# Optimization experiments

Measured on AMD Instinct MI355X. Metric: run time of the kernel, lower is better.

Reference implementation:

```python
import jax, jax.numpy as jnp
import numpy as np

G, S, DG, HN, HE, L, F = 64, 160, 128, 128, 16, 2, 16


def _rn(k, shape, scale=0.05):
    return jax.random.normal(k, shape, dtype=jnp.float32) * scale


def setup_inputs() -> dict:
    ks = jax.random.split(jax.random.key(0), 26)
    return {
        "gene_codes": jax.random.normal(ks[0], (G, DG), dtype=jnp.float32),
        "node_entry_w": _rn(ks[1], (HN, DG)), "node_entry_b": _rn(ks[2], (HN,)),
        "node_wih0": _rn(ks[3], (4 * HN, 1)), "node_wih": _rn(ks[4], (L - 1, 4 * HN, HN)),
        "node_whh": _rn(ks[5], (L, 4 * HN, HN)), "node_bih": _rn(ks[6], (L, 4 * HN)), "node_bhh": _rn(ks[7], (L, 4 * HN)),
        "node_exit_w": _rn(ks[8], (32, HN)), "node_exit_b": _rn(ks[9], (32,)),
        "edge_entry_w": _rn(ks[10], (HE, 32)), "edge_entry_b": _rn(ks[11], (HE,)),
        "edge_wih0": _rn(ks[12], (4 * HE, 1)), "edge_wih": _rn(ks[13], (L - 1, 4 * HE, HE)),
        "edge_whh": _rn(ks[14], (L, 4 * HE, HE)), "edge_bih": _rn(ks[15], (L, 4 * HE)), "edge_bhh": _rn(ks[16], (L, 4 * HE)),
        "ee1_w": _rn(ks[17], (8, HE)), "ee1_b": _rn(ks[18], (8,)),
        "ee2_w": _rn(ks[19], (2, 8)), "ee2_b": _rn(ks[20], (2,)),
        "ef1_w": _rn(ks[21], (8, HE)), "ef1_b": _rn(ks[22], (8,)),
        "ef2_w": _rn(ks[23], (2 * F, 8)), "ef2_b": _rn(ks[24], (2 * F,)),
        "graphs_size": S,
    }


def _lstm_zero_input(h0, wih0, wih, whh, bih, bhh, steps):
    # Multi-layer PyTorch-style LSTM (gate order i,f,g,o) whose input sequence is all-zeros
    # of feature size 1; h0 is replicated across layers (as in the original .repeat).
    nl = whh.shape[0]
    h = jnp.stack([h0] * nl)
    c = jnp.zeros_like(h)
    zero_in = jnp.zeros((h0.shape[0], 1), h0.dtype)

    def step(carry, _):
        h, c = carry
        hs, cs = [], []
        inp = zero_in
        for l in range(nl):
            w_in = wih0 if l == 0 else wih[l - 1]
            gates = inp @ w_in.T + h[l] @ whh[l].T + bih[l] + bhh[l]
            i, f, g, o = jnp.split(gates, 4, axis=-1)
            cn = jax.nn.sigmoid(f) * c[l] + jax.nn.sigmoid(i) * jnp.tanh(g)
            hn = jax.nn.sigmoid(o) * jnp.tanh(cn)
            hs.append(hn); cs.append(cn)
            inp = hn
        return (jnp.stack(hs), jnp.stack(cs)), hs[-1]

    _, outs = jax.lax.scan(step, (h, c), None, length=steps)
    return outs  # [steps, B, H] top-layer hiddens


def reference(gene_codes, node_entry_w, node_entry_b, node_wih0, node_wih, node_whh, node_bih, node_bhh, node_exit_w, node_exit_b, edge_entry_w, edge_entry_b, edge_wih0, edge_wih, edge_whh, edge_bih, edge_bhh, ee1_w, ee1_b, ee2_w, ee2_b, ef1_w, ef1_b, ef2_w, ef2_b, graphs_size):
    s_len = int(graphs_size)
    g_n = gene_codes.shape[0]
    n_max = s_len + 1
    m = s_len * g_n  # total node steps == number of edge sequences
    fdim = ef2_w.shape[0] // 2

    # node RNN over zero inputs, h0 from gene codes
    h0n = jax.nn.relu(gene_codes @ node_entry_w.T + node_entry_b)
    node_out = _lstm_zero_input(h0n, node_wih0, node_wih, node_whh, node_bih, node_bhh, s_len)  # [S,G,HN]
    # uniform graph sizes: torch's flipped packed data == reversed step-major layout,
    # flat index k -> (step = S-1-k//G, graph = k%G)
    node_flat = jnp.flip(node_out, axis=0).reshape(m, -1)

    # edge RNN: one sequence per node step; zero inputs, so full-length run gives
    # identical hiddens at every valid packed step
    h0e = jax.nn.relu(jax.nn.relu(node_flat @ node_exit_w.T + node_exit_b) @ edge_entry_w.T + edge_entry_b)
    eh = _lstm_zero_input(h0e, edge_wih0, edge_wih, edge_whh, edge_bih, edge_bhh, s_len)  # [S,M,HE]

    e = jax.nn.sigmoid(jax.nn.relu(eh @ ee1_w.T + ee1_b) @ ee2_w.T + ee2_b)          # [S,M,2]
    f = (jax.nn.relu(eh @ ef1_w.T + ef1_b) @ ef2_w.T + ef2_b).reshape(s_len, m, 2, fdim)

    # ragged index construction: edge sequence k has row = edges_size[k] = S - k//G,
    # graph id = k%G, valid steps s < row, column = s
    k = jnp.arange(m)
    gid = k % g_n
    row = s_len - k // g_n
    s = jnp.arange(s_len)[:, None]
    mask = (s < row[None, :]).reshape(-1)
    gid2 = jnp.broadcast_to(gid[None, :], (s_len, m)).reshape(-1)
    row2 = jnp.broadcast_to(row[None, :], (s_len, m)).reshape(-1)
    col2 = jnp.broadcast_to(s, (s_len, m)).reshape(-1)

    el = jnp.where(mask, e[..., 0].reshape(-1), 0.0)
    eu = jnp.where(mask, e[..., 1].reshape(-1), 0.0)
    exist = jnp.zeros((g_n, n_max, n_max), gene_codes.dtype)
    exist = exist.at[gid2, row2, col2].add(el).at[gid2, col2, row2].add(eu)

    fl = jnp.where(mask[:, None], f[:, :, 0, :].reshape(-1, fdim), 0.0)
    fu = jnp.where(mask[:, None], f[:, :, 1, :].reshape(-1, fdim), 0.0)
    feat = jnp.zeros((g_n, n_max, n_max, fdim), gene_codes.dtype)
    feat = feat.at[gid2, row2, col2].add(fl).at[gid2, col2, row2].add(fu)
    return exist, feat
```

## Files before the change

### kernel.cpp

```cpp
#include <hip/hip_runtime.h>


typedef __attribute__((ext_vector_type(8))) short short8;
typedef __attribute__((ext_vector_type(4))) short short4v;
typedef __attribute__((ext_vector_type(4))) float floatx4;
typedef _Float16 half2v __attribute__((ext_vector_type(2)));

#define NG 64
#define NMAX 161
#define CH 16
#define NCH 10

__device__ __forceinline__ float sgm(float x) {
  return __builtin_amdgcn_rcpf(1.0f + __expf(-x));
}
__device__ __forceinline__ float tanhf_(float x) {
  return 2.0f * __builtin_amdgcn_rcpf(1.0f + __expf(-2.0f * x)) - 1.0f;
}
__device__ __forceinline__ unsigned short f2b(float x) {
  union { float f; unsigned u; } v; v.f = x;
  unsigned r = v.u + 0x7fffu + ((v.u >> 16) & 1u);
  return (unsigned short)(r >> 16);
}
__device__ __forceinline__ float b2f(unsigned short h) {
  union { unsigned u; float f; } v; v.u = ((unsigned)h) << 16; return v.f;
}
__device__ __forceinline__ half2v pkh(float a, float b) {
  return __builtin_bit_cast(half2v, __builtin_amdgcn_cvt_pkrtz(a, b));
}
__device__ __forceinline__ void barrier_lds() {
  asm volatile("s_waitcnt lgkmcnt(0)" ::: "memory");
  __builtin_amdgcn_s_barrier();
}

#define RORF(x, N) __builtin_bit_cast(float, __builtin_amdgcn_update_dpp(      \
    __builtin_bit_cast(int, (x)), __builtin_bit_cast(int, (x)),                \
    0x120 | (N), 0xF, 0xF, false))

__device__ __forceinline__ void rotpack(float h, half2v* out) {
  const float r1  = RORF(h, 1),  r2  = RORF(h, 2),  r3  = RORF(h, 3);
  const float r4  = RORF(h, 4),  r5  = RORF(h, 5),  r6  = RORF(h, 6);
  const float r7  = RORF(h, 7),  r8  = RORF(h, 8),  r9  = RORF(h, 9);
  const float r10 = RORF(h, 10), r11 = RORF(h, 11), r12 = RORF(h, 12);
  const float r13 = RORF(h, 13), r14 = RORF(h, 14), r15 = RORF(h, 15);
  out[0] = pkh(h,   r1);
  out[1] = pkh(r2,  r3);
  out[2] = pkh(r4,  r5);
  out[3] = pkh(r6,  r7);
  out[4] = pkh(r8,  r9);
  out[5] = pkh(r10, r11);
  out[6] = pkh(r12, r13);
  out[7] = pkh(r14, r15);
}

__global__ __launch_bounds__(512) void node_fused(
    const float* __restrict__ gene,
    const float* __restrict__ entw,
    const float* __restrict__ entb,
    const float* __restrict__ nwih,
    const float* __restrict__ nwhh,
    const float* __restrict__ nbih,
    const float* __restrict__ nbhh,
    unsigned short* __restrict__ h0w,
    unsigned short* __restrict__ X3,
    unsigned short* __restrict__ nflat,
    int* __restrict__ flag0, int* __restrict__ flag1)
{
  __shared__ __align__(16) unsigned short hA[2][16][136];
  __shared__ __align__(16) unsigned short s_b[128][136];

  const int tid  = threadIdx.x;
  const int role = blockIdx.x >> 2;
  const int rb4  = blockIdx.x & 3;
  const int wv   = tid >> 6;
  const int lane = tid & 63;
  const int lo   = lane & 15;
  const int hi   = lane >> 4;

  if (role == 0) {
    const int nb = rb4;
    const int u  = (wv << 4) | lo;

    short8 B0[4][4];
#pragma unroll
    for (int t = 0; t < 4; ++t) {
      const int n = t * 128 + u;
#pragma unroll
      for (int ks = 0; ks < 4; ++ks) {
        const float* src = nwhh + n * 128 + ks * 32 + hi * 8;
        short8 bfr;
#pragma unroll
        for (int jj = 0; jj < 8; ++jj) bfr[jj] = (short)f2b(src[jj]);
        B0[t][ks] = bfr;
      }
    }
    const float bi0 = nbih[u]       + nbhh[u];
    const float bf0 = nbih[128 + u] + nbhh[128 + u];
    const float bg0 = nbih[256 + u] + nbhh[256 + u];
    const float bo0 = nbih[384 + u] + nbhh[384 + u];

    {
      const int q  = tid >> 5;
      const int u4 = (tid & 31) * 4;
      const float* gc = gene + (nb * 16 + q) * 128;
      float acc[4] = { entb[u4], entb[u4 + 1], entb[u4 + 2], entb[u4 + 3] };
      for (int qq = 0; qq < 32; ++qq) {
        const float4 gv = *(const float4*)&gc[qq * 4];
#pragma unroll
        for (int r = 0; r < 4; ++r) {
          const float4 wv2 = *(const float4*)&entw[(u4 + r) * 128 + qq * 4];
          acc[r] += gv.x * wv2.x + gv.y * wv2.y + gv.z * wv2.z + gv.w * wv2.w;
        }
      }
#pragma unroll
      for (int r = 0; r < 4; ++r)
        hA[0][q][u4 + r] = f2b(fmaxf(acc[r], 0.0f));
    }

    float c0[4] = {0.f, 0.f, 0.f, 0.f};
    __syncthreads();

    for (int c = 0; c < NCH; ++c) {
      for (int tt = 0; tt < CH; ++tt) {
        const int t  = c * CH + tt;
        const int rb = t & 1, wb = rb ^ 1;
        floatx4 a0 = {bi0, bi0, bi0, bi0};
        floatx4 a1 = {bf0, bf0, bf0, bf0};
        floatx4 a2 = {bg0, bg0, bg0, bg0};
        floatx4 a3 = {bo0, bo0, bo0, bo0};
        const unsigned short* ar = &hA[rb][lo][hi * 8];
#pragma unroll
        for (int ks = 0; ks < 4; ++ks) {
          const short8 afr = *(const short8*)(ar + ks * 32);
          a0 = __builtin_amdgcn_mfma_f32_16x16x32_bf16(afr, B0[0][ks], a0, 0, 0, 0);
          a1 = __builtin_amdgcn_mfma_f32_16x16x32_bf16(afr, B0[1][ks], a1, 0, 0, 0);
          a2 = __builtin_amdgcn_mfma_f32_16x16x32_bf16(afr, B0[2][ks], a2, 0, 0, 0);
          a3 = __builtin_amdgcn_mfma_f32_16x16x32_bf16(afr, B0[3][ks], a3, 0, 0, 0);
        }
        const size_t obase = (size_t)(t * 64 + nb * 16) * 128;
#pragma unroll
        for (int r = 0; r < 4; ++r) {
          const float iv = sgm(a0[r]);
          const float fv = sgm(a1[r]);
          const float gv = tanhf_(a2[r]);
          const float ov = sgm(a3[r]);
          const float cn = fv * c0[r] + iv * gv;
          c0[r] = cn;
          const unsigned short hb = f2b(ov * tanhf_(cn));
          const int q = hi * 4 + r;
          hA[wb][q][u] = hb;
          __builtin_nontemporal_store(hb, &h0w[obase + (size_t)q * 128 + u]);
        }
        if (tt < CH - 1) barrier_lds();
      }
      __syncthreads();
      if (tid == 0) {
        __threadfence();
        __hip_atomic_fetch_add(&flag0[c], 1, __ATOMIC_RELEASE,
                               __HIP_MEMORY_SCOPE_AGENT);
      }
    }

  } else if (role == 1) {
    const int xg = rb4;
    for (int i = tid; i < 128 * 32; i += 512) {
      const int nc = i >> 5, k4 = (i & 31) * 4;
      const float4 w = *(const float4*)&nwih[(size_t)(xg * 128 + nc) * 128 + k4];
      s_b[nc][k4]     = f2b(w.x);
      s_b[nc][k4 + 1] = f2b(w.y);
      s_b[nc][k4 + 2] = f2b(w.z);
      s_b[nc][k4 + 3] = f2b(w.w);
    }
    const int gg = wv & 3;
    const int ch = wv >> 2;

    for (int c = 0; c < NCH; ++c) {
      if (tid == 0) {
        while (__hip_atomic_load(&flag0[c], __ATOMIC_ACQUIRE,
                                 __HIP_MEMORY_SCOPE_AGENT) < 4)
          __builtin_amdgcn_s_sleep(8);
        __threadfence();
      }
      __syncthreads();

      for (int tt = 0; tt < CH; ++tt) {
        const int t = c * CH + tt;
        floatx4 acc[4];
#pragma unroll
        for (int nt = 0; nt < 4; ++nt) acc[nt] = (floatx4){0.f, 0.f, 0.f, 0.f};
        const unsigned short* arow =
            h0w + (size_t)(t * 64 + gg * 16 + lo) * 128 + hi * 8;
#pragma unroll
        for (int ks = 0; ks < 4; ++ks) {
          const short8 afr = *(const short8*)(arow + ks * 32);
#pragma unroll
          for (int nt = 0; nt < 4; ++nt) {
            const short8 bfr =
                *(const short8*)&s_b[ch * 64 + nt * 16 + lo][ks * 32 + hi * 8];
            acc[nt] = __builtin_amdgcn_mfma_f32_16x16x32_bf16(afr, bfr, acc[nt], 0, 0, 0);
          }
        }
#pragma unroll
        for (int nt = 0; nt < 4; ++nt) {
          const size_t base3 =
              ((((size_t)gg * 160 + t) * 512) + xg * 128 + ch * 64 + nt * 16 + lo) * 16
              + hi * 4;
          short4v xv;
#pragma unroll
          for (int r = 0; r < 4; ++r) xv[r] = (short)f2b(acc[nt][r]);
          __builtin_nontemporal_store(xv, (short4v*)&X3[base3]);
        }
      }
      __syncthreads();
      if (tid == 0) {
        __threadfence();
        __hip_atomic_fetch_add(&flag1[c], 1, __ATOMIC_RELEASE,
                               __HIP_MEMORY_SCOPE_AGENT);
      }
    }

  } else {
    const int nb = rb4;
    const int u  = (wv << 4) | lo;

    short8 B1[4][4];
#pragma unroll
    for (int t = 0; t < 4; ++t) {
      const int n = t * 128 + u;
#pragma unroll
      for (int ks = 0; ks < 4; ++ks) {
        const float* src = nwhh + 512 * 128 + n * 128 + ks * 32 + hi * 8;
        short8 bfr;
#pragma unroll
        for (int jj = 0; jj < 8; ++jj) bfr[jj] = (short)f2b(src[jj]);
        B1[t][ks] = bfr;
      }
    }
    const float bi1 = nbih[512 + u]       + nbhh[512 + u];
    const float bf1 = nbih[512 + 128 + u] + nbhh[512 + 128 + u];
    const float bg1 = nbih[512 + 256 + u] + nbhh[512 + 256 + u];
    const float bo1 = nbih[512 + 384 + u] + nbhh[512 + 384 + u];

    {
      const int q  = tid >> 5;
      const int u4 = (tid & 31) * 4;
      const float* gc = gene + (nb * 16 + q) * 128;
      float acc[4] = { entb[u4], entb[u4 + 1], entb[u4 + 2], entb[u4 + 3] };
      for (int qq = 0; qq < 32; ++qq) {
        const float4 gv = *(const float4*)&gc[qq * 4];
#pragma unroll
        for (int r = 0; r < 4; ++r) {
          const float4 wv2 = *(const float4*)&entw[(u4 + r) * 128 + qq * 4];
          acc[r] += gv.x * wv2.x + gv.y * wv2.y + gv.z * wv2.z + gv.w * wv2.w;
        }
      }
#pragma unroll
      for (int r = 0; r < 4; ++r)
        hA[0][q][u4 + r] = f2b(fmaxf(acc[r], 0.0f));
    }

    float c1[4] = {0.f, 0.f, 0.f, 0.f};
    const size_t xstep = 512 * 16;
    const unsigned short* xb = X3 + ((size_t)nb * 160) * xstep
                             + (size_t)u * 16 + hi * 4;
    __syncthreads();

    for (int c = 0; c < NCH; ++c) {
      if (tid == 0) {
        while (__hip_atomic_load(&flag1[c], __ATOMIC_ACQUIRE,
                                 __HIP_MEMORY_SCOPE_AGENT) < 4)
          __builtin_amdgcn_s_sleep(8);
        __threadfence();
      }
      __syncthreads();

      const unsigned short* xp = xb + (size_t)(c * CH) * xstep;
      short4v x0 = *(const short4v*)(xp);
      short4v x1 = *(const short4v*)(xp + 128 * 16);
      short4v x2 = *(const short4v*)(xp + 256 * 16);
      short4v x3 = *(const short4v*)(xp + 384 * 16);

      for (int tt = 0; tt < CH; ++tt) {
        const int t  = c * CH + tt;
        const int rb = t & 1, wb = rb ^ 1;

        floatx4 a0 = {bi1, bi1, bi1, bi1};
        floatx4 a1 = {bf1, bf1, bf1, bf1};
        floatx4 a2 = {bg1, bg1, bg1, bg1};
        floatx4 a3 = {bo1, bo1, bo1, bo1};
        const unsigned short* ar = &hA[rb][lo][hi * 8];
#pragma unroll
        for (int ks = 0; ks < 4; ++ks) {
          const short8 afr = *(const short8*)(ar + ks * 32);
          a0 = __builtin_amdgcn_mfma_f32_16x16x32_bf16(afr, B1[0][ks], a0, 0, 0, 0);
          a1 = __builtin_amdgcn_mfma_f32_16x16x32_bf16(afr, B1[1][ks], a1, 0, 0, 0);
          a2 = __builtin_amdgcn_mfma_f32_16x16x32_bf16(afr, B1[2][ks], a2, 0, 0, 0);
          a3 = __builtin_amdgcn_mfma_f32_16x16x32_bf16(afr, B1[3][ks], a3, 0, 0, 0);
        }

        const short4v cx0 = x0, cx1 = x1, cx2 = x2, cx3 = x3;
        if (tt + 1 < CH) {
          const unsigned short* xn = xb + (size_t)(t + 1) * xstep;
          x0 = *(const short4v*)(xn);
          x1 = *(const short4v*)(xn + 128 * 16);
          x2 = *(const short4v*)(xn + 256 * 16);
          x3 = *(const short4v*)(xn + 384 * 16);
        }

        const size_t obase = (size_t)((159 - t) * 64 + nb * 16) * 128;
#pragma unroll
        for (int r = 0; r < 4; ++r) {
          const float iv = sgm(a0[r] + b2f((unsigned short)cx0[r]));
          const float fv = sgm(a1[r] + b2f((unsigned short)cx1[r]));
          const float gv = tanhf_(a2[r] + b2f((unsigned short)cx2[r]));
          const float ov = sgm(a3[r] + b2f((unsigned short)cx3[r]));
          const float cn = fv * c1[r] + iv * gv;
          c1[r] = cn;
          const unsigned short hb = f2b(ov * tanhf_(cn));
          const int q = hi * 4 + r;
          hA[wb][q][u] = hb;
          __builtin_nontemporal_store(hb, &nflat[obase + (size_t)q * 128 + u]);
        }
        barrier_lds();
      }
    }
  }
}

__global__ __launch_bounds__(256, 1) void edge_kernel(
    const unsigned short* __restrict__ nflat,
    const float* __restrict__ exw, const float* __restrict__ exb,
    const float* __restrict__ enw, const float* __restrict__ enb,
    const float* __restrict__ ewih,
    const float* __restrict__ ewhh,
    const float* __restrict__ ebih, const float* __restrict__ ebhh,
    const float* __restrict__ ee1w, const float* __restrict__ ee1b,
    const float* __restrict__ ee2w, const float* __restrict__ ee2b,
    const float* __restrict__ ef1w, const float* __restrict__ ef1b,
    const float* __restrict__ ef2w, const float* __restrict__ ef2b,
    float* __restrict__ out)
{
  const int tid = threadIdx.x;
  const int sg  = tid >> 4;
  const int u   = tid & 15;
  const int b   = blockIdx.x;

  const int row = b >> 8, r = b & 255;
  const int bb  = (row == 1) ? (511 - r) : ((row << 8) + r);
  const int kbase = bb * 16;
  const int jrow  = 160 - (bb >> 2);
  const int gid   = (kbase & 63) + sg;

  __shared__ __align__(16) float s_nf[16][132];
  __shared__ float s_w0s[64][17];
  __shared__ float s_was[64][17];
  __shared__ float s_wbs[64][17];
  __shared__ float s_wh[16][17];
  __shared__ float s_ef2[32][10];
  __shared__ __align__(16) float s_ee2[16];
  __shared__ __align__(16) float t1b[16][12];
  __shared__ __align__(16) float t2b[16][12];
  __shared__ __align__(16) float x32[16][36];

  for (int i = tid; i < 16 * 128; i += 256)
    s_nf[i >> 7][i & 127] = b2f(nflat[(size_t)(kbase + (i >> 7)) * 128 + (i & 127)]);
  for (int i = tid; i < 64 * 16; i += 256) {
    s_w0s[i >> 4][i & 15] = ewhh[i];
    s_was[i >> 4][i & 15] = ewih[i];
    s_wbs[i >> 4][i & 15] = ewhh[1024 + i];
  }
  for (int i = tid; i < 8 * 16; i += 256) {
    s_wh[i >> 4][i & 15]       = ee1w[i];
    s_wh[8 + (i >> 4)][i & 15] = ef1w[i];
  }
  for (int i = tid; i < 32 * 8; i += 256) s_ef2[i >> 3][i & 7] = ef2w[i];
  if (tid < 16) s_ee2[tid] = ee2w[tid];

  if (b < NG) {
    for (int d = tid; d < NMAX; d += 256) {
      out[(size_t)b * (NMAX * NMAX) + (size_t)d * NMAX + d] = 0.0f;
      float* fb = out + (size_t)NG * NMAX * NMAX
                + ((size_t)b * NMAX * NMAX + (size_t)d * NMAX + d) * 16;
#pragma unroll
      for (int q = 0; q < 16; ++q) fb[q] = 0.0f;
    }
  }

  const float be0i = ebih[u]      + ebhh[u];
  const float be0f = ebih[16 + u] + ebhh[16 + u];
  const float be0g = ebih[32 + u] + ebhh[32 + u];
  const float be0o = ebih[48 + u] + ebhh[48 + u];
  const float be1i = ebih[64 + u]      + ebhh[64 + u];
  const float be1f = ebih[64 + 16 + u] + ebhh[64 + 16 + u];
  const float be1g = ebih[64 + 32 + u] + ebhh[64 + 32 + u];
  const float be1o = ebih[64 + 48 + u] + ebhh[64 + 48 + u];
  const float hbias = (u < 8) ? ee1b[u] : ef1b[u - 8];
  const float f2bl = ef2b[u], f2bu = ef2b[16 + u];
  const float e2bias = (u < 2) ? ee2b[u] : 0.0f;

  __syncthreads();

  half2v W0h[4][8], WAh[4][8], WBh[4][8], WHh[8];
#pragma unroll
  for (int g = 0; g < 4; ++g) {
    const int rw = g * 16 + u;
#pragma unroll
    for (int j = 0; j < 8; ++j) {
      const int v0 = (u + 2 * j) & 15, v1 = (u + 2 * j + 1) & 15;
      W0h[g][j] = pkh(s_w0s[rw][v0], s_w0s[rw][v1]);
      WAh[g][j] = pkh(s_was[rw][v0], s_was[rw][v1]);
      WBh[g][j] = pkh(s_wbs[rw][v0], s_wbs[rw][v1]);
    }
  }
#pragma unroll
  for (int j = 0; j < 8; ++j) {
    const int v0 = (u + 2 * j) & 15, v1 = (u + 2 * j + 1) & 15;
    WHh[j] = pkh(s_wh[u][v0], s_wh[u][v1]);
  }

  {
    float acc0 = exb[u], acc1 = exb[16 + u];
    const float* w0p = exw + u * 128;
    const float* w1p = exw + (16 + u) * 128;
    for (int qq = 0; qq < 32; ++qq) {
      const float4 nv  = *(const float4*)&s_nf[sg][qq * 4];
      const float4 w0v = *(const float4*)&w0p[qq * 4];
      const float4 w1v = *(const float4*)&w1p[qq * 4];
      acc0 += nv.x * w0v.x + nv.y * w0v.y + nv.z * w0v.z + nv.w * w0v.w;
      acc1 += nv.x * w1v.x + nv.y * w1v.y + nv.z * w1v.z + nv.w * w1v.w;
    }
    x32[sg][u] = fmaxf(acc0, 0.0f);
    x32[sg][16 + u] = fmaxf(acc1, 0.0f);
  }
  __builtin_amdgcn_wave_barrier();
  float c0 = 0.0f, c1 = 0.0f;
  half2v h20[8], h21[8];
  {
    float acc = enb[u];
    const float* ewp = enw + u * 32;
#pragma unroll
    for (int qq = 0; qq < 8; ++qq) {
      const float4 xv  = *(const float4*)&x32[sg][qq * 4];
      const float4 wv2 = *(const float4*)&ewp[qq * 4];
      acc += xv.x * wv2.x + xv.y * wv2.y + xv.z * wv2.z + xv.w * wv2.w;
    }
    const float h0e = fmaxf(acc, 0.0f);
    rotpack(h0e, h20);
#pragma unroll
    for (int j = 0; j < 8; ++j) h21[j] = h20[j];
  }

  float* exi = out + (size_t)gid * (NMAX * NMAX);
  float* fea = out + (size_t)NG * NMAX * NMAX + (size_t)gid * (NMAX * NMAX) * 16;
  const int jN = jrow * NMAX;

  for (int s = 0; s <= jrow; ++s) {
    const bool doStep = (s < jrow);
    const bool doHead = (s > 0);

    float a0, a1, a2, a3;
    if (doStep) {
      a0 = be0i; a1 = be0f; a2 = be0g; a3 = be0o;
#pragma unroll
      for (int j = 0; j < 8; ++j) {
        a0 = __builtin_amdgcn_fdot2(h20[j], W0h[0][j], a0, false);
        a1 = __builtin_amdgcn_fdot2(h20[j], W0h[1][j], a1, false);
        a2 = __builtin_amdgcn_fdot2(h20[j], W0h[2][j], a2, false);
        a3 = __builtin_amdgcn_fdot2(h20[j], W0h[3][j], a3, false);
      }
    }

    if (doHead) {
      __builtin_amdgcn_wave_barrier();
      const int sm = s - 1;
      const float2 ta0 = *(const float2*)&t2b[sg][0];
      const float2 ta1 = *(const float2*)&t2b[sg][2];
      const float2 ta2 = *(const float2*)&t2b[sg][4];
      const float2 ta3 = *(const float2*)&t2b[sg][6];
      const float2 wl0 = *(const float2*)&s_ef2[u][0];
      const float2 wl1 = *(const float2*)&s_ef2[u][2];
      const float2 wl2 = *(const float2*)&s_ef2[u][4];
      const float2 wl3 = *(const float2*)&s_ef2[u][6];
      const float2 wu0 = *(const float2*)&s_ef2[16 + u][0];
      const float2 wu1 = *(const float2*)&s_ef2[16 + u][2];
      const float2 wu2 = *(const float2*)&s_ef2[16 + u][4];
      const float2 wu3 = *(const float2*)&s_ef2[16 + u][6];
      const float fl = f2bl
          + ta0.x * wl0.x + ta0.y * wl0.y + ta1.x * wl1.x + ta1.y * wl1.y
          + ta2.x * wl2.x + ta2.y * wl2.y + ta3.x * wl3.x + ta3.y * wl3.y;
      const float fu = f2bu
          + ta0.x * wu0.x + ta0.y * wu0.y + ta1.x * wu1.x + ta1.y * wu1.y
          + ta2.x * wu2.x + ta2.y * wu2.y + ta3.x * wu3.x + ta3.y * wu3.y;
      fea[((size_t)jN + sm) * 16 + u] = fl;
      fea[((size_t)sm * NMAX + jrow) * 16 + u] = fu;
      if (u < 2) {
        const float4 t1a = *(const float4*)&t1b[sg][0];
        const float4 t1c = *(const float4*)&t1b[sg][4];
        const float4 we0 = *(const float4*)&s_ee2[u * 8];
        const float4 we1 = *(const float4*)&s_ee2[u * 8 + 4];
        float e = e2bias
            + t1a.x * we0.x + t1a.y * we0.y + t1a.z * we0.z + t1a.w * we0.w
            + t1c.x * we1.x + t1c.y * we1.y + t1c.z * we1.z + t1c.w * we1.w;
        const size_t idx = (u == 0) ? ((size_t)jN + sm)
                                    : ((size_t)sm * NMAX + jrow);
        exi[idx] = sgm(e);
      }
    }

    if (doStep) {
      {
        const float iv = sgm(a0), fv = sgm(a1), gv = tanhf_(a2), ov = sgm(a3);
        c0 = fv * c0 + iv * gv;
        rotpack(ov * tanhf_(c0), h20);
      }
      float b0 = be1i, b1 = be1f, b2 = be1g, b3 = be1o;
#pragma unroll
      for (int j = 0; j < 8; ++j) {
        b0 = __builtin_amdgcn_fdot2(h20[j], WAh[0][j], b0, false);
        b1 = __builtin_amdgcn_fdot2(h20[j], WAh[1][j], b1, false);
        b2 = __builtin_amdgcn_fdot2(h20[j], WAh[2][j], b2, false);
        b3 = __builtin_amdgcn_fdot2(h20[j], WAh[3][j], b3, false);
      }
#pragma unroll
      for (int j = 0; j < 8; ++j) {
        b0 = __builtin_amdgcn_fdot2(h21[j], WBh[0][j], b0, false);
        b1 = __builtin_amdgcn_fdot2(h21[j], WBh[1][j], b1, false);
        b2 = __builtin_amdgcn_fdot2(h21[j], WBh[2][j], b2, false);
        b3 = __builtin_amdgcn_fdot2(h21[j], WBh[3][j], b3, false);
      }
      {
        const float iv = sgm(b0), fv = sgm(b1), gv = tanhf_(b2), ov = sgm(b3);
        c1 = fv * c1 + iv * gv;
        rotpack(ov * tanhf_(c1), h21);
      }
      {
        float th = hbias;
#pragma unroll
        for (int j = 0; j < 8; ++j)
          th = __builtin_amdgcn_fdot2(h21[j], WHh[j], th, false);
        th = fmaxf(th, 0.0f);
        if (u < 8) t1b[sg][u] = th; else t2b[sg][u - 8] = th;
      }
      __builtin_amdgcn_wave_barrier();
    }
  }
}

extern "C" void kernel_launch(void* const* d_in, const int* in_sizes, int n_in,
                              void* d_out, int out_size, void* d_ws, size_t ws_size,
                              hipStream_t stream) {
  (void)in_sizes; (void)n_in; (void)out_size; (void)ws_size;
  const float* gene = (const float*)d_in[0];
  const float* entw = (const float*)d_in[1];
  const float* entb = (const float*)d_in[2];
  const float* nwih = (const float*)d_in[4];
  const float* nwhh = (const float*)d_in[5];
  const float* nbih = (const float*)d_in[6];
  const float* nbhh = (const float*)d_in[7];
  const float* exw  = (const float*)d_in[8];
  const float* exb  = (const float*)d_in[9];
  const float* enw  = (const float*)d_in[10];
  const float* enb  = (const float*)d_in[11];
  const float* ewih = (const float*)d_in[13];
  const float* ewhh = (const float*)d_in[14];
  const float* ebih = (const float*)d_in[15];
  const float* ebhh = (const float*)d_in[16];
  const float* ee1w = (const float*)d_in[17];
  const float* ee1b = (const float*)d_in[18];
  const float* ee2w = (const float*)d_in[19];
  const float* ee2b = (const float*)d_in[20];
  const float* ef1w = (const float*)d_in[21];
  const float* ef1b = (const float*)d_in[22];
  const float* ef2w = (const float*)d_in[23];
  const float* ef2b = (const float*)d_in[24];

  char* ws = (char*)d_ws;
  unsigned short* nflat = (unsigned short*)(ws);
  unsigned short* h0w   = (unsigned short*)(ws + 2621440);
  int* flag0            = (int*)(ws + 5242880);
  int* flag1            = (int*)(ws + 5242880 + 4096);
  unsigned short* X3    = (unsigned short*)(ws + 5259264);

  hipMemsetAsync(ws + 5242880, 0, 8192, stream);
  node_fused<<<12, 512, 0, stream>>>(gene, entw, entb, nwih, nwhh, nbih, nbhh,
                                     h0w, X3, nflat, flag0, flag1);
  edge_kernel<<<640, 256, 0, stream>>>(nflat, exw, exb, enw, enb, ewih, ewhh,
                                       ebih, ebhh, ee1w, ee1b, ee2w, ee2b,
                                       ef1w, ef1b, ef2w, ef2b, (float*)d_out);
}
```

Baseline: 459.0 us.

## Fuse layer-1 input projection into layer-0 recurrence blocks, drop middle role

Each layer-0 block now keeps the full layer-1 input weight matrix in LDS (about 136 KB). After each step it multiplies its fresh hidden state by that matrix and writes X3 directly. This removes the intermediate h0 buffer, the separate projection role and one stage of cross-block flag handoff. The layer-1 blocks now wait on a per-block counter instead of a per-chunk counter. In exchange, the layer-0 recurrence does extra MFMA work and a barrier on its serial critical path every step, and the large LDS allocation limits occupancy.

New measurement: 456.4 us. No clear change (-0.6%).

```diff
diff --git a/kernel.cpp b/kernel.cpp
--- a/kernel.cpp
+++ b/kernel.cpp
@@ -61,25 +61,34 @@
     const float* __restrict__ nwhh,
     const float* __restrict__ nbih,
     const float* __restrict__ nbhh,
-    unsigned short* __restrict__ h0w,
     unsigned short* __restrict__ X3,
     unsigned short* __restrict__ nflat,
-    int* __restrict__ flag0, int* __restrict__ flag1)
+    int* __restrict__ flagP)
 {
-  __shared__ __align__(16) unsigned short hA[2][16][136];
-  __shared__ __align__(16) unsigned short s_b[128][136];
-
   const int tid  = threadIdx.x;
   const int role = blockIdx.x >> 2;
-  const int rb4  = blockIdx.x & 3;
+  const int nb   = blockIdx.x & 3;
   const int wv   = tid >> 6;
   const int lane = tid & 63;
   const int lo   = lane & 15;
   const int hi   = lane >> 4;
 
+  if (role == 1) return;
+
+  __shared__ __align__(16) unsigned short hA[2][16][136];
+
   if (role == 0) {
-    const int nb = rb4;
-    const int u  = (wv << 4) | lo;
+    __shared__ __align__(16) unsigned short s_wih[512][136];
+    const int u = (wv << 4) | lo;
+
+    for (int i = tid; i < 512 * 32; i += 512) {
+      const int nc = i >> 5, k4 = (i & 31) * 4;
+      const float4 w = *(const float4*)&nwih[(size_t)nc * 128 + k4];
+      s_wih[nc][k4]     = f2b(w.x);
+      s_wih[nc][k4 + 1] = f2b(w.y);
+      s_wih[nc][k4 + 2] = f2b(w.z);
+      s_wih[nc][k4 + 3] = f2b(w.w);
+    }
 
     short8 B0[4][4];
 #pragma unroll
@@ -137,7 +146,6 @@
           a2 = __builtin_amdgcn_mfma_f32_16x16x32_bf16(afr, B0[2][ks], a2, 0, 0, 0);
           a3 = __builtin_amdgcn_mfma_f32_16x16x32_bf16(afr, B0[3][ks], a3, 0, 0, 0);
         }
-        const size_t obase = (size_t)(t * 64 + nb * 16) * 128;
 #pragma unroll
         for (int r = 0; r < 4; ++r) {
           const float iv = sgm(a0[r]);
@@ -146,82 +154,37 @@
           const float ov = sgm(a3[r]);
           const float cn = fv * c0[r] + iv * gv;
           c0[r] = cn;
-          const unsigned short hb = f2b(ov * tanhf_(cn));
-          const int q = hi * 4 + r;
-          hA[wb][q][u] = hb;
-          __builtin_nontemporal_store(hb, &h0w[obase + (size_t)q * 128 + u]);
-        }
-        if (tt < CH - 1) barrier_lds();
+          hA[wb][hi * 4 + r][u] = f2b(ov * tanhf_(cn));
+        }
+        barrier_lds();
+        const unsigned short* axr = &hA[wb][lo][hi * 8];
+        const size_t xrow = ((size_t)(nb * 160 + t)) * (512 * 16);
+#pragma unroll
+        for (int ct = 0; ct < 4; ++ct) {
+          const int colb = (wv * 4 + ct) * 16;
+          floatx4 xa = {0.f, 0.f, 0.f, 0.f};
+#pragma unroll
+          for (int ks = 0; ks < 4; ++ks) {
+            const short8 afr = *(const short8*)(axr + ks * 32);
+            const short8 bfr = *(const short8*)&s_wih[colb + lo][ks * 32 + hi * 8];
+            xa = __builtin_amdgcn_mfma_f32_16x16x32_bf16(afr, bfr, xa, 0, 0, 0);
+          }
+          short4v xv;
+#pragma unroll
+          for (int r = 0; r < 4; ++r) xv[r] = (short)f2b(xa[r]);
+          *(short4v*)&X3[xrow + (size_t)(colb + lo) * 16 + hi * 4] = xv;
+        }
       }
       __syncthreads();
       if (tid == 0) {
         __threadfence();
-        __hip_atomic_fetch_add(&flag0[c], 1, __ATOMIC_RELEASE,
+        __hip_atomic_fetch_add(&flagP[nb], 1, __ATOMIC_RELEASE,
                                __HIP_MEMORY_SCOPE_AGENT);
       }
     }
 
-  } else if (role == 1) {
-    const int xg = rb4;
-    for (int i = tid; i < 128 * 32; i += 512) {
-      const int nc = i >> 5, k4 = (i & 31) * 4;
-      const float4 w = *(const float4*)&nwih[(size_t)(xg * 128 + nc) * 128 + k4];
-      s_b[nc][k4]     = f2b(w.x);
-      s_b[nc][k4 + 1] = f2b(w.y);
-      s_b[nc][k4 + 2] = f2b(w.z);
-      s_b[nc][k4 + 3] = f2b(w.w);
-    }
-    const int gg = wv & 3;
-    const int ch = wv >> 2;
-
-    for (int c = 0; c < NCH; ++c) {
-      if (tid == 0) {
-        while (__hip_atomic_load(&flag0[c], __ATOMIC_ACQUIRE,
-                                 __HIP_MEMORY_SCOPE_AGENT) < 4)
-          __builtin_amdgcn_s_sleep(8);
-        __threadfence();
-      }
-      __syncthreads();
-
-      for (int tt = 0; tt < CH; ++tt) {
-        const int t = c * CH + tt;
-        floatx4 acc[4];
-#pragma unroll
-        for (int nt = 0; nt < 4; ++nt) acc[nt] = (floatx4){0.f, 0.f, 0.f, 0.f};
-        const unsigned short* arow =
-            h0w + (size_t)(t * 64 + gg * 16 + lo) * 128 + hi * 8;
-#pragma unroll
-        for (int ks = 0; ks < 4; ++ks) {
-          const short8 afr = *(const short8*)(arow + ks * 32);
-#pragma unroll
-          for (int nt = 0; nt < 4; ++nt) {
-            const short8 bfr =
-                *(const short8*)&s_b[ch * 64 + nt * 16 + lo][ks * 32 + hi * 8];
-            acc[nt] = __builtin_amdgcn_mfma_f32_16x16x32_bf16(afr, bfr, acc[nt], 0, 0, 0);
-          }
-        }
-#pragma unroll
-        for (int nt = 0; nt < 4; ++nt) {
-          const size_t base3 =
-              ((((size_t)gg * 160 + t) * 512) + xg * 128 + ch * 64 + nt * 16 + lo) * 16
-              + hi * 4;
-          short4v xv;
-#pragma unroll
-          for (int r = 0; r < 4; ++r) xv[r] = (short)f2b(acc[nt][r]);
-          __builtin_nontemporal_store(xv, (short4v*)&X3[base3]);
-        }
-      }
-      __syncthreads();
-      if (tid == 0) {
-        __threadfence();
-        __hip_atomic_fetch_add(&flag1[c], 1, __ATOMIC_RELEASE,
-                               __HIP_MEMORY_SCOPE_AGENT);
-      }
-    }
-
   } else {
-    const int nb = rb4;
-    const int u  = (wv << 4) | lo;
+    const int u = (wv << 4) | lo;
 
     short8 B1[4][4];
 #pragma unroll
@@ -267,8 +230,8 @@
 
     for (int c = 0; c < NCH; ++c) {
       if (tid == 0) {
-        while (__hip_atomic_load(&flag1[c], __ATOMIC_ACQUIRE,
-                                 __HIP_MEMORY_SCOPE_AGENT) < 4)
+        while (__hip_atomic_load(&flagP[nb], __ATOMIC_ACQUIRE,
+                                 __HIP_MEMORY_SCOPE_AGENT) < c + 1)
           __builtin_amdgcn_s_sleep(8);
         __threadfence();
       }
@@ -319,7 +282,7 @@
           const unsigned short hb = f2b(ov * tanhf_(cn));
           const int q = hi * 4 + r;
           hA[wb][q][u] = hb;
-          __builtin_nontemporal_store(hb, &nflat[obase + (size_t)q * 128 + u]);
+          nflat[obase + (size_t)q * 128 + u] = hb;
         }
         barrier_lds();
       }
@@ -576,14 +539,12 @@
 
   char* ws = (char*)d_ws;
   unsigned short* nflat = (unsigned short*)(ws);
-  unsigned short* h0w   = (unsigned short*)(ws + 2621440);
-  int* flag0            = (int*)(ws + 5242880);
-  int* flag1            = (int*)(ws + 5242880 + 4096);
-  unsigned short* X3    = (unsigned short*)(ws + 5259264);
-
-  hipMemsetAsync(ws + 5242880, 0, 8192, stream);
+  unsigned short* X3    = (unsigned short*)(ws + 2621440);
+  int* flagP            = (int*)(ws + 13107200);
+
+  hipMemsetAsync(ws + 13107200, 0, 4096, stream);
   node_fused<<<12, 512, 0, stream>>>(gene, entw, entb, nwih, nwhh, nbih, nbhh,
-                                     h0w, X3, nflat, flag0, flag1);
+                                     X3, nflat, flagP);
   edge_kernel<<<640, 256, 0, stream>>>(nflat, exw, exb, enw, enb, ewih, ewhh,
                                        ebih, ebhh, ee1w, ee1b, ee2w, ee2b,
                                        ef1w, ef1b, ef2w, ef2b, (float*)d_out);
```
